# Kernel tuning notes

Measured on AMD Instinct MI355X. Metric: run time of the kernel, lower is better.

Reference implementation:

```python
import jax, jax.numpy as jnp
import numpy as np
import math
from jax import lax

DIM = 128
D_STATE = 16
D_CONV = 4
EXPAND = 2
NSLICES = 16
D_INNER = EXPAND * DIM          # 256
DT_RANK = math.ceil(DIM / 16)   # 8
B_, H_, W_ = 4, 64, 64
L = H_ * W_                     # 4096


def silu(x):
    return x * jax.nn.sigmoid(x)


def causal_conv1d(x, w, b):
    # x: (b, d, l), w: (d, k) depthwise, b: (d,)  -- causal, output length l
    l = x.shape[-1]
    xp = jnp.pad(x, ((0, 0), (0, 0), (D_CONV - 1, 0)))
    y = sum(w[None, :, k, None] * xp[:, :, k:k + l] for k in range(D_CONV))
    return y + b[None, :, None]


def selective_scan(u, delta, A, B, C):
    # u, delta: (b, d, l); A: (d, n); B, C: (b, n, l)
    bsz, d, l = u.shape
    n = A.shape[1]
    u_t = u.transpose(2, 0, 1)      # (l, b, d)
    d_t = delta.transpose(2, 0, 1)  # (l, b, d)
    B_t = B.transpose(2, 0, 1)      # (l, b, n)
    C_t = C.transpose(2, 0, 1)      # (l, b, n)

    def step(h, inp):
        u_, de_, b_, c_ = inp
        dA = jnp.exp(de_[..., None] * A)                    # (b, d, n)
        h = h * dA + (de_ * u_)[..., None] * b_[:, None, :]  # (b, d, n)
        y = jnp.einsum('bdn,bn->bd', h, c_)
        return h, y

    h0 = jnp.zeros((bsz, d, n), u.dtype)
    _, ys = lax.scan(step, h0, (u_t, d_t, B_t, C_t))
    return ys.transpose(1, 2, 0)  # (b, d, l)


def mamba_dir(xz, conv_w, conv_b, x_proj_w, dt_w, dt_b, A_log, Dp):
    # one directional Mamba branch (conv + S6 scan + silu(z) gating), returns (b, d_inner, l)
    x, z = jnp.split(xz, 2, axis=1)
    x = silu(causal_conv1d(x, conv_w, conv_b))
    x_dbl = jnp.einsum('rd,bdl->brl', x_proj_w, x)          # (b, dt_rank+2n, l)
    dt_raw = x_dbl[:, :DT_RANK]
    Bm = x_dbl[:, DT_RANK:DT_RANK + D_STATE]
    Cm = x_dbl[:, DT_RANK + D_STATE:]
    delta = jax.nn.softplus(jnp.einsum('dr,brl->bdl', dt_w, dt_raw) + dt_b[None, :, None])
    A = -jnp.exp(A_log)
    y = selective_scan(x, delta, A, Bm, Cm)
    y = y + Dp[None, :, None] * x
    return y * silu(z)


def setup_inputs() -> dict:
    key = jax.random.key(0)
    ks = iter(jax.random.split(key, 40))

    def rn(shape, scale=0.02):
        return jax.random.normal(next(ks), shape, dtype=jnp.float32) * scale

    inp = {"x_in": jax.random.normal(next(ks), (B_, H_, W_, DIM), dtype=jnp.float32)}
    inp["in_proj_w"] = rn((2 * D_INNER, DIM))
    for suf in ["", "_b", "_s"]:
        inp["conv_w" + suf] = rn((D_INNER, D_CONV), 0.1)
        inp["conv_b" + suf] = rn((D_INNER,), 0.1)
        inp["x_proj_w" + suf] = rn((DT_RANK + 2 * D_STATE, D_INNER))
        inp["dt_proj_w" + suf] = rn((D_INNER, DT_RANK), 0.1)
        inp["dt_proj_b" + suf] = rn((D_INNER,), 0.1)
        inp["A_log" + suf] = jnp.log(jnp.tile(jnp.arange(1, D_STATE + 1, dtype=jnp.float32), (D_INNER, 1)))
        inp["D" + suf] = jnp.ones((D_INNER,), jnp.float32)
    inp["out_proj_w"] = rn((DIM, D_INNER))
    return inp


def reference(x_in, in_proj_w, conv_w, conv_b, x_proj_w, dt_proj_w, dt_proj_b, A_log, D,
              conv_w_b, conv_b_b, x_proj_w_b, dt_proj_w_b, dt_proj_b_b, A_log_b, D_b,
              conv_w_s, conv_b_s, x_proj_w_s, dt_proj_w_s, dt_proj_b_s, A_log_s, D_s,
              out_proj_w):
    b, h, w, c = x_in.shape
    l = h * w
    x = x_in.reshape(b, l, c)
    xz = jnp.einsum('pd,bld->bpl', in_proj_w, x)  # (b, 2*d_inner, l)

    # forward scan
    y_f = mamba_dir(xz, conv_w, conv_b, x_proj_w, dt_proj_w, dt_proj_b, A_log, D)
    # backward scan (flip along length)
    y_b = jnp.flip(mamba_dir(jnp.flip(xz, -1), conv_w_b, conv_b_b, x_proj_w_b,
                             dt_proj_w_b, dt_proj_b_b, A_log_b, D_b), -1)
    # interleaved-slice scan: chunk length into NSLICES pieces, stack, flatten
    m = l // NSLICES
    xz_s = xz.reshape(b, 2 * D_INNER, NSLICES, m).swapaxes(-1, -2).reshape(b, 2 * D_INNER, l)
    y_s = mamba_dir(xz_s, conv_w_s, conv_b_s, x_proj_w_s, dt_proj_w_s, dt_proj_b_s, A_log_s, D_s)
    y_s = y_s.reshape(b, D_INNER, m, NSLICES).swapaxes(-1, -2).reshape(b, D_INNER, l)

    y = y_f + y_b + y_s
    out = jnp.einsum('od,bdl->blo', out_proj_w, y)
    return out.reshape(b, h, w, c)
```

## Files before the change

kernel.cpp:

```cpp
#include <hip/hip_runtime.h>
#include <math.h>

#define LSEQ 4096

#define XZ_OFF   0ULL
#define XZ_SZ    (4ULL * 4096 * 512)
#define U_OFF    (XZ_OFF + XZ_SZ)
#define DIR_SZ   (4ULL * 256 * 4096)
#define DELTA_OFF (U_OFF + 3ULL * DIR_SZ)
#define BC_OFF   (DELTA_OFF + 3ULL * DIR_SZ)
#define BC_SZ    (4ULL * 4096 * 32)
#define WTIN_OFF DELTA_OFF
#define WTOUT_OFF U_OFF

typedef float v2f __attribute__((ext_vector_type(2)));
typedef float v4f __attribute__((ext_vector_type(4)));

__device__ __forceinline__ float sigmoidf_(float x) { return 1.0f / (1.0f + __expf(-x)); }
__device__ __forceinline__ float siluf_(float x)    { return x * sigmoidf_(x); }

__device__ __forceinline__ float fast_exp2_asm(float x) {
    float r;
    asm volatile("v_exp_f32 %0, %1\n\ts_nop 0" : "=v"(r) : "v"(x));
    return r;
}
#if defined(__has_builtin)
#if __has_builtin(__builtin_amdgcn_exp2f)
#define EXP2(x) __builtin_amdgcn_exp2f(x)
#else
#define EXP2(x) fast_exp2_asm(x)
#endif
#else
#define EXP2(x) fast_exp2_asm(x)
#endif

__device__ __forceinline__ float softplus_fast(float x) {
    float t = EXP2(1.44269504f * x);
    float r = 0.69314718f * __log2f(1.0f + t);
    return (x > 20.0f) ? x : r;
}

__device__ __forceinline__ int perm_idx(int dir, int j) {
    if (dir == 0) return j;
    if (dir == 1) return 4095 - j;
    return ((j & 15) << 8) | (j >> 4);
}

#define DPP_MOV(x, ctrl) __int_as_float(__builtin_amdgcn_update_dpp(0, __float_as_int(x), (ctrl), 0xF, 0xF, true))

__global__ __launch_bounds__(256) void transpose_in_kernel(const float* __restrict__ w,
                                                           float* __restrict__ wT) {
    int idx = blockIdx.x * 256 + threadIdx.x;
    int p = idx >> 7, c = idx & 127;
    wT[(size_t)c * 512 + p] = w[(size_t)p * 128 + c];
}

__global__ __launch_bounds__(256) void inproj_kernel(const float* __restrict__ x,
                              const float* __restrict__ wT,
                              float* __restrict__ xz) {
    const int b = blockIdx.y;
    const int l0 = blockIdx.x * 16;
    __shared__ float xs[128 * 20];
    for (int idx = threadIdx.x; idx < 16 * 128; idx += 256) {
        int li = idx >> 7, c = idx & 127;
        xs[c * 20 + li] = x[((size_t)(b * 4096 + l0 + li)) * 128 + c];
    }
    __syncthreads();
    const int p0 = (threadIdx.x & 127) * 4;
    const int g8 = (threadIdx.x >> 7) * 8;
    float acc[4][8];
    #pragma unroll
    for (int j = 0; j < 4; ++j)
        #pragma unroll
        for (int k = 0; k < 8; ++k) acc[j][k] = 0.0f;
    for (int c = 0; c < 128; ++c) {
        float4 wv = *(const float4*)(wT + (size_t)c * 512 + p0);
        const float* xp = xs + c * 20 + g8;
        float4 x0 = *(const float4*)(xp);
        float4 x1 = *(const float4*)(xp + 4);
        float xv[8] = {x0.x, x0.y, x0.z, x0.w, x1.x, x1.y, x1.z, x1.w};
        float wj[4] = {wv.x, wv.y, wv.z, wv.w};
        #pragma unroll
        for (int j = 0; j < 4; ++j)
            #pragma unroll
            for (int k = 0; k < 8; ++k) acc[j][k] += wj[j] * xv[k];
    }
    #pragma unroll
    for (int k = 0; k < 8; ++k) {
        float4 s; s.x = acc[0][k]; s.y = acc[1][k]; s.z = acc[2][k]; s.w = acc[3][k];
        *(float4*)(xz + ((size_t)(b * 4096 + l0 + g8 + k)) * 512 + p0) = s;
    }
}

__global__ __launch_bounds__(256) void front_kernel(float* __restrict__ ws,
        const float* __restrict__ xw0, const float* __restrict__ xw1, const float* __restrict__ xw2,
        const float* __restrict__ dw0, const float* __restrict__ dw1, const float* __restrict__ dw2,
        const float* __restrict__ db0, const float* __restrict__ db1, const float* __restrict__ db2,
        const float* __restrict__ cw0, const float* __restrict__ cb0,
        const float* __restrict__ cw1, const float* __restrict__ cb1,
        const float* __restrict__ cw2, const float* __restrict__ cb2) {
    const int l0 = blockIdx.x * 32, b = blockIdx.y, dir = blockIdx.z;
    const float* xw = (dir == 0) ? xw0 : (dir == 1) ? xw1 : xw2;
    const float* dw = (dir == 0) ? dw0 : (dir == 1) ? dw1 : dw2;
    const float* db = (dir == 0) ? db0 : (dir == 1) ? db1 : db2;
    const float* cw = (dir == 0) ? cw0 : (dir == 1) ? cw1 : cw2;
    const float* cb = (dir == 0) ? cb0 : (dir == 1) ? cb1 : cb2;
    const float* xzb = ws + XZ_OFF + (size_t)b * 4096 * 512;
    float* ub      = ws + U_OFF + (size_t)dir * DIR_SZ + (size_t)b * 256 * 4096;
    float* deltab  = ws + DELTA_OFF + (size_t)dir * DIR_SZ + (size_t)b * 256 * 4096;
    float* Bf      = ws + BC_OFF + (size_t)dir * BC_SZ;
    float* Cf      = Bf + BC_SZ / 2;

    __shared__ float xt[35 * 260];
    __shared__ float xd[40 * 33];
    __shared__ float xws[40 * 68];
    float* ut = xt;

    for (int idx = threadIdx.x; idx < 35 * 64; idx += 256) {
        int k = idx >> 6, dq = idx & 63;
        int j = l0 - 3 + k;
        float4 v = {0.f, 0.f, 0.f, 0.f};
        if (j >= 0) {
            int row = (dir == 0) ? j : (dir == 1) ? (4095 - j) : (((j & 15) << 8) | (j >> 4));
            v = *(const float4*)(xzb + (size_t)row * 512 + dq * 4);
        }
        *(float4*)(xt + k * 260 + dq * 4) = v;
    }
    __syncthreads();

    const int d = threadIdx.x;
    const float w0 = cw[d * 4 + 0], w1 = cw[d * 4 + 1], w2 = cw[d * 4 + 2], w3 = cw[d * 4 + 3];
    const float bb = cb[d];
    float win[35];
    #pragma unroll
    for (int k = 0; k < 35; ++k) win[k] = xt[k * 260 + d];
    float r[32];
    #pragma unroll
    for (int li = 0; li < 32; ++li)
        r[li] = siluf_(bb + w0 * win[li] + w1 * win[li + 1] + w2 * win[li + 2] + w3 * win[li + 3]);
    {
        float* urow = ub + (size_t)d * 4096 + l0;
        #pragma unroll
        for (int q = 0; q < 8; ++q) {
            float4 v; v.x = r[q*4]; v.y = r[q*4+1]; v.z = r[q*4+2]; v.w = r[q*4+3];
            *(float4*)(urow + q * 4) = v;
        }
    }
    __syncthreads();

    #pragma unroll
    for (int li = 0; li < 32; ++li)
        ut[li * 264 + 4 * (((d >> 2) ^ (li & 7))) + (d & 3)] = r[li];

    {
        const int rg = threadIdx.x >> 5;
        const int li = threadIdx.x & 31;
        float acc[5];
        #pragma unroll
        for (int j = 0; j < 5; ++j) acc[j] = 0.0f;
        const float* up = ut + li * 264;
        const int sw = (li & 7);
        for (int ct = 0; ct < 4; ++ct) {
            __syncthreads();
            for (int idx = threadIdx.x; idx < 40 * 16; idx += 256) {
                int rr = idx >> 4, q = (idx & 15) * 4;
                *(float4*)(xws + rr * 68 + q) = *(const float4*)(xw + (size_t)rr * 256 + ct * 64 + q);
            }
            __syncthreads();
            #pragma unroll 4
            for (int c4t = 0; c4t < 16; ++c4t) {
                const int cc = 4 * (c4t ^ sw);
                float4 uv = *(const float4*)(up + ct * 64 + cc);
                #pragma unroll
                for (int j = 0; j < 5; ++j) {
                    float4 wv = *(const float4*)(xws + (rg * 5 + j) * 68 + cc);
                    acc[j] += wv.x * uv.x + wv.y * uv.y + wv.z * uv.z + wv.w * uv.w;
                }
            }
        }
        #pragma unroll
        for (int j = 0; j < 5; ++j) xd[(rg * 5 + j) * 33 + li] = acc[j];
    }
    __syncthreads();

    {
        const int wv = threadIdx.x >> 6;
        const int lane = threadIdx.x & 63;
        const int n = lane >> 2, lq = lane & 3;
        #pragma unroll
        for (int j = 0; j < 2; ++j) {
            int l4 = (l0 >> 2) + j * 4 + wv;
            int li = (j * 4 + wv) * 4 + lq;
            size_t base = (((size_t)b * 1024 + l4) * 16 + n) * 4 + lq;
            Bf[base] = xd[(8 + n) * 33 + li];
            Cf[base] = xd[(24 + n) * 33 + li];
        }
    }
    {
        const int li = threadIdx.x & 31;
        float xr8[8];
        #pragma unroll
        for (int rr = 0; rr < 8; ++rr) xr8[rr] = xd[rr * 33 + li];
        #pragma unroll
        for (int k = 0; k < 32; ++k) {
            int dd = ((threadIdx.x + k * 256) >> 5);
            float4 wa = *(const float4*)(dw + dd * 8);
            float4 wb = *(const float4*)(dw + dd * 8 + 4);
            float acc = db[dd]
                + wa.x * xr8[0] + wa.y * xr8[1] + wa.z * xr8[2] + wa.w * xr8[3]
                + wb.x * xr8[4] + wb.y * xr8[5] + wb.z * xr8[6] + wb.w * xr8[7];
            deltab[(size_t)dd * 4096 + l0 + li] = softplus_fast(acc);
        }
    }
}

__global__ __launch_bounds__(512) void scan_kernel(float* __restrict__ ws,
                            const float* __restrict__ Al0, const float* __restrict__ Dp0,
                            const float* __restrict__ Al1, const float* __restrict__ Dp1,
                            const float* __restrict__ Al2, const float* __restrict__ Dp2) {
    const int d = blockIdx.x, b = blockIdx.y, dir = blockIdx.z;
    const float* Al = (dir == 0) ? Al0 : (dir == 1) ? Al1 : Al2;
    const float* Dp = (dir == 0) ? Dp0 : (dir == 1) ? Dp1 : Dp2;
    const int c = threadIdx.x >> 4;
    const int n = threadIdx.x & 15;
    const int qid = n >> 2;
    const float Ane = -1.44269504f * __expf(Al[d * 16 + n]);
    const v2f AneD = {Ane, Ane};
    const float Dd = Dp[d];
    const float* urow = ws + U_OFF + (size_t)dir * DIR_SZ + ((size_t)(b * 256 + d)) * 4096;
    float* drow = ws + DELTA_OFF + (size_t)dir * DIR_SZ + ((size_t)(b * 256 + d)) * 4096;

    __shared__ float sdu[32 * 260];
    __shared__ float red[32 * 34];
    float* Psh = red;
    float* Ssh = red + 512;

    {
        const float4* d4 = (const float4*)drow;
        const float4* u4 = (const float4*)urow;
        for (int i = threadIdx.x; i < 1024; i += 512) {
            float4 dv = d4[i], uv = u4[i];
            int l = i * 4;
            float* p = sdu + (l >> 7) * 260 + (l & 127) * 2;
            float4 du;
            du.x = dv.x * uv.x; du.y = dv.y * uv.y; du.z = dv.z * uv.z; du.w = dv.w * uv.w;
            *(float4*)(p) = dv; *(float4*)(p + 4) = du;
        }
    }
    __syncthreads();

    const v4f* Bq = (const v4f*)(ws + BC_OFF + (size_t)dir * BC_SZ)
                       + ((size_t)b * 1024 + c * 32) * 16 + n;
    const v4f* Cq = (const v4f*)(ws + BC_OFF + (size_t)dir * BC_SZ + BC_SZ / 2)
                       + ((size_t)b * 1024 + c * 32) * 16 + n;
    const v4f* sp = (const v4f*)(sdu + c * 260);

    float S = 0.0f;
    v2f ds2 = {0.0f, 0.0f};
    #pragma unroll 8
    for (int k4 = 0; k4 < 32; ++k4) {
        v4f dq = sp[k4 * 2], uq = sp[k4 * 2 + 1];
        v4f Bv = Bq[(size_t)k4 * 16];
        v2f t0 = AneD * dq.xy;
        v2f t1 = AneD * dq.zw;
        v2f p0 = uq.xy * Bv.xy;
        v2f p1 = uq.zw * Bv.zw;
        ds2 += dq.xy + dq.zw;
        S = __builtin_fmaf(S, EXP2(t0.x), p0.x);
        S = __builtin_fmaf(S, EXP2(t0.y), p0.y);
        S = __builtin_fmaf(S, EXP2(t1.x), p1.x);
        S = __builtin_fmaf(S, EXP2(t1.y), p1.y);
    }
    Ssh[c * 16 + n] = S;
    Psh[c * 16 + n] = EXP2(Ane * (ds2.x + ds2.y));
    __syncthreads();
    float h = 0.0f;
    for (int k = 0; k < c; ++k) h = h * Psh[k * 16 + n] + Ssh[k * 16 + n];
    __syncthreads();

    #define SCAN_STEP(t, ee, pp, Cn) { \
        h = __builtin_fmaf(h, (ee), (pp)); \
        float yp = h * (Cn); \
        yp += DPP_MOV(yp, 0xB1); \
        yp += DPP_MOV(yp, 0x4E); \
        red[(4 * (t) + qid) * 34 + c] = yp; }

    for (int g = 0; g < 16; ++g) {
        v4f d0 = sp[g * 4 + 0], u0 = sp[g * 4 + 1];
        v4f d1 = sp[g * 4 + 2], u1 = sp[g * 4 + 3];
        v4f Bv0 = Bq[(size_t)(g * 2) * 16], Bv1 = Bq[(size_t)(g * 2 + 1) * 16];
        v4f Cv0 = Cq[(size_t)(g * 2) * 16], Cv1 = Cq[(size_t)(g * 2 + 1) * 16];
        v2f t0 = AneD * d0.xy, t1 = AneD * d0.zw;
        v2f t2 = AneD * d1.xy, t3 = AneD * d1.zw;
        v2f p0 = u0.xy * Bv0.xy, p1 = u0.zw * Bv0.zw;
        v2f p2 = u1.xy * Bv1.xy, p3 = u1.zw * Bv1.zw;
        float e0 = EXP2(t0.x), e1 = EXP2(t0.y);
        float e2 = EXP2(t1.x), e3 = EXP2(t1.y);
        float e4 = EXP2(t2.x), e5 = EXP2(t2.y);
        float e6 = EXP2(t3.x), e7 = EXP2(t3.y);
        SCAN_STEP(0, e0, p0.x, Cv0.x)
        SCAN_STEP(1, e1, p0.y, Cv0.y)
        SCAN_STEP(2, e2, p1.x, Cv0.z)
        SCAN_STEP(3, e3, p1.y, Cv0.w)
        SCAN_STEP(4, e4, p2.x, Cv1.x)
        SCAN_STEP(5, e5, p2.y, Cv1.y)
        SCAN_STEP(6, e6, p3.x, Cv1.z)
        SCAN_STEP(7, e7, p3.y, Cv1.w)
        const int tt = n & 7;
        float q0 = red[(4 * tt + 0) * 34 + c];
        float q1 = red[(4 * tt + 1) * 34 + c];
        float q2 = red[(4 * tt + 2) * 34 + c];
        float q3 = red[(4 * tt + 3) * 34 + c];
        float y = (q0 + q1) + (q2 + q3);
        if (n < 8) {
            int gl = c * 128 + g * 8 + n;
            drow[perm_idx(dir, gl)] = y + Dd * urow[gl];
        }
    }
    #undef SCAN_STEP
}

__global__ __launch_bounds__(256) void transpose_w_kernel(const float* __restrict__ ow,
                                                          float* __restrict__ wT) {
    int idx = blockIdx.x * 256 + threadIdx.x;
    int o = idx >> 8, d = idx & 255;
    wT[(size_t)d * 128 + o] = ow[(size_t)o * 256 + d];
}

__global__ __launch_bounds__(256) void epilogue_kernel(const float* __restrict__ ws,
                                const float* __restrict__ wT,
                                float* __restrict__ out) {
    const int l0 = blockIdx.x * 16, b = blockIdx.y;
    __shared__ float yt[256 * 20];
    __shared__ float wts[64 * 128];
    const float* yf = ws + DELTA_OFF;
    const float* yb = ws + DELTA_OFF + DIR_SZ;
    const float* ysd = ws + DELTA_OFF + 2 * DIR_SZ;
    const float* xzb = ws + XZ_OFF + (size_t)b * 4096 * 512;

    for (int idx = threadIdx.x; idx < 256 * 4; idx += 256) {
        int d = idx >> 2, q = (idx & 3) * 4;
        size_t ro = ((size_t)(b * 256 + d)) * 4096 + l0 + q;
        float4 vf = *(const float4*)(yf + ro);
        float4 vb = *(const float4*)(yb + ro);
        float4 vs = *(const float4*)(ysd + ro);
        float4 s; s.x = vf.x + vb.x + vs.x; s.y = vf.y + vb.y + vs.y;
        s.z = vf.z + vb.z + vs.z; s.w = vf.w + vb.w + vs.w;
        *(float4*)(yt + d * 20 + q) = s;
    }
    __syncthreads();
    {
        const int d = threadIdx.x;
        #pragma unroll 4
        for (int li = 0; li < 16; ++li) {
            float z = xzb[(size_t)(l0 + li) * 512 + 256 + d];
            yt[d * 20 + li] *= siluf_(z);
        }
    }

    const int o0 = (threadIdx.x & 31) * 4;
    const int lp = (threadIdx.x >> 5) * 2;
    float a0[4], a1[4];
    #pragma unroll
    for (int j = 0; j < 4; ++j) { a0[j] = 0.0f; a1[j] = 0.0f; }
    for (int dt = 0; dt < 4; ++dt) {
        __syncthreads();
        for (int idx = threadIdx.x; idx < 64 * 32; idx += 256) {
            int dd = idx >> 5, q = (idx & 31) * 4;
            *(float4*)(wts + dd * 128 + q) = *(const float4*)(wT + (size_t)(dt * 64 + dd) * 128 + q);
        }
        __syncthreads();
        #pragma unroll 4
        for (int dl = 0; dl < 64; ++dl) {
            float4 w = *(const float4*)(wts + dl * 128 + o0);
            float2 y = *(const float2*)(yt + (dt * 64 + dl) * 20 + lp);
            a0[0] += w.x * y.x; a0[1] += w.y * y.x; a0[2] += w.z * y.x; a0[3] += w.w * y.x;
            a1[0] += w.x * y.y; a1[1] += w.y * y.y; a1[2] += w.z * y.y; a1[3] += w.w * y.y;
        }
    }
    float4 s0; s0.x = a0[0]; s0.y = a0[1]; s0.z = a0[2]; s0.w = a0[3];
    float4 s1; s1.x = a1[0]; s1.y = a1[1]; s1.z = a1[2]; s1.w = a1[3];
    *(float4*)(out + ((size_t)(b * 4096 + l0 + lp)) * 128 + o0) = s0;
    *(float4*)(out + ((size_t)(b * 4096 + l0 + lp + 1)) * 128 + o0) = s1;
}

extern "C" void kernel_launch(void* const* d_in, const int* in_sizes, int n_in,
                              void* d_out, int out_size, void* d_ws, size_t ws_size,
                              hipStream_t stream) {
    const float* x_in = (const float*)d_in[0];
    const float* ipw  = (const float*)d_in[1];
    const float* cw[3]  = {(const float*)d_in[2],  (const float*)d_in[9],  (const float*)d_in[16]};
    const float* cb[3]  = {(const float*)d_in[3],  (const float*)d_in[10], (const float*)d_in[17]};
    const float* xpw[3] = {(const float*)d_in[4],  (const float*)d_in[11], (const float*)d_in[18]};
    const float* dtw[3] = {(const float*)d_in[5],  (const float*)d_in[12], (const float*)d_in[19]};
    const float* dtb[3] = {(const float*)d_in[6],  (const float*)d_in[13], (const float*)d_in[20]};
    const float* alog[3]= {(const float*)d_in[7],  (const float*)d_in[14], (const float*)d_in[21]};
    const float* dp[3]  = {(const float*)d_in[8],  (const float*)d_in[15], (const float*)d_in[22]};
    const float* ow   = (const float*)d_in[23];
    float* ws  = (float*)d_ws;
    float* out = (float*)d_out;

    transpose_in_kernel<<<dim3(256), 256, 0, stream>>>(ipw, ws + WTIN_OFF);
    inproj_kernel<<<dim3(256, 4), 256, 0, stream>>>(x_in, ws + WTIN_OFF, ws);
    front_kernel<<<dim3(128, 4, 3), 256, 0, stream>>>(ws,
        xpw[0], xpw[1], xpw[2], dtw[0], dtw[1], dtw[2], dtb[0], dtb[1], dtb[2],
        cw[0], cb[0], cw[1], cb[1], cw[2], cb[2]);
    scan_kernel<<<dim3(256, 4, 3), 512, 0, stream>>>(ws,
        alog[0], dp[0], alog[1], dp[1], alog[2], dp[2]);
    transpose_w_kernel<<<dim3(128), 256, 0, stream>>>(ow, ws + WTOUT_OFF);
    epilogue_kernel<<<dim3(256, 4), 256, 0, stream>>>(ws, ws + WTOUT_OFF, out);
}
```

Baseline: 379.0 us.

## Replace LDS reduction in scan with full DPP row reduction and lane select

In the scan kernel the sum over the 16 state lanes now uses four DPP adds instead of writing partial sums to a shared reduction buffer and reading them back. Each lane keeps the output for its own timestep in a register, so the shared buffer and the barrier after the chunk-prefix loop can be removed. The kernel also stores raw u rather than delta*u in LDS and reads u for the skip term from LDS instead of global memory, with a minimum-blocks hint added to launch bounds. The cost is extra DPP and multiply work per step, which is traded for fewer LDS accesses and less synchronisation.

```diff
diff --git a/kernel.cpp b/kernel.cpp
--- a/kernel.cpp
+++ b/kernel.cpp
@@ -214,7 +214,7 @@
     }
 }
 
-__global__ __launch_bounds__(512) void scan_kernel(float* __restrict__ ws,
+__global__ __launch_bounds__(512, 8) void scan_kernel(float* __restrict__ ws,
                             const float* __restrict__ Al0, const float* __restrict__ Dp0,
                             const float* __restrict__ Al1, const float* __restrict__ Dp1,
                             const float* __restrict__ Al2, const float* __restrict__ Dp2) {
@@ -223,7 +223,7 @@
     const float* Dp = (dir == 0) ? Dp0 : (dir == 1) ? Dp1 : Dp2;
     const int c = threadIdx.x >> 4;
     const int n = threadIdx.x & 15;
-    const int qid = n >> 2;
+    const int nl = n & 7;
     const float Ane = -1.44269504f * __expf(Al[d * 16 + n]);
     const v2f AneD = {Ane, Ane};
     const float Dd = Dp[d];
@@ -231,9 +231,9 @@
     float* drow = ws + DELTA_OFF + (size_t)dir * DIR_SZ + ((size_t)(b * 256 + d)) * 4096;
 
     __shared__ float sdu[32 * 260];
-    __shared__ float red[32 * 34];
-    float* Psh = red;
-    float* Ssh = red + 512;
+    __shared__ float ps[1024];
+    float* Psh = ps;
+    float* Ssh = ps + 512;
 
     {
         const float4* d4 = (const float4*)drow;
@@ -242,9 +242,7 @@
             float4 dv = d4[i], uv = u4[i];
             int l = i * 4;
             float* p = sdu + (l >> 7) * 260 + (l & 127) * 2;
-            float4 du;
-            du.x = dv.x * uv.x; du.y = dv.y * uv.y; du.z = dv.z * uv.z; du.w = dv.w * uv.w;
-            *(float4*)(p) = dv; *(float4*)(p + 4) = du;
+            *(float4*)(p) = dv; *(float4*)(p + 4) = uv;
         }
     }
     __syncthreads();
@@ -261,10 +259,12 @@
     for (int k4 = 0; k4 < 32; ++k4) {
         v4f dq = sp[k4 * 2], uq = sp[k4 * 2 + 1];
         v4f Bv = Bq[(size_t)k4 * 16];
+        v2f du0 = dq.xy * uq.xy;
+        v2f du1 = dq.zw * uq.zw;
         v2f t0 = AneD * dq.xy;
         v2f t1 = AneD * dq.zw;
-        v2f p0 = uq.xy * Bv.xy;
-        v2f p1 = uq.zw * Bv.zw;
+        v2f p0 = du0 * Bv.xy;
+        v2f p1 = du1 * Bv.zw;
         ds2 += dq.xy + dq.zw;
         S = __builtin_fmaf(S, EXP2(t0.x), p0.x);
         S = __builtin_fmaf(S, EXP2(t0.y), p0.y);
@@ -275,29 +275,36 @@
     Psh[c * 16 + n] = EXP2(Ane * (ds2.x + ds2.y));
     __syncthreads();
     float h = 0.0f;
-    for (int k = 0; k < c; ++k) h = h * Psh[k * 16 + n] + Ssh[k * 16 + n];
-    __syncthreads();
+    #pragma unroll 2
+    for (int k = 0; k < c; ++k) h = __builtin_fmaf(h, Psh[k * 16 + n], Ssh[k * 16 + n]);
 
     #define SCAN_STEP(t, ee, pp, Cn) { \
         h = __builtin_fmaf(h, (ee), (pp)); \
         float yp = h * (Cn); \
         yp += DPP_MOV(yp, 0xB1); \
         yp += DPP_MOV(yp, 0x4E); \
-        red[(4 * (t) + qid) * 34 + c] = yp; }
+        yp += DPP_MOV(yp, 0x124); \
+        yp += DPP_MOV(yp, 0x128); \
+        if (nl == (t)) ysel = yp; }
 
     for (int g = 0; g < 16; ++g) {
+        const int j0 = g * 8 + nl;
+        float uo = sdu[c * 260 + ((j0 >> 2) << 3) + 4 + (j0 & 3)];
         v4f d0 = sp[g * 4 + 0], u0 = sp[g * 4 + 1];
         v4f d1 = sp[g * 4 + 2], u1 = sp[g * 4 + 3];
         v4f Bv0 = Bq[(size_t)(g * 2) * 16], Bv1 = Bq[(size_t)(g * 2 + 1) * 16];
         v4f Cv0 = Cq[(size_t)(g * 2) * 16], Cv1 = Cq[(size_t)(g * 2 + 1) * 16];
         v2f t0 = AneD * d0.xy, t1 = AneD * d0.zw;
         v2f t2 = AneD * d1.xy, t3 = AneD * d1.zw;
-        v2f p0 = u0.xy * Bv0.xy, p1 = u0.zw * Bv0.zw;
-        v2f p2 = u1.xy * Bv1.xy, p3 = u1.zw * Bv1.zw;
+        v2f q0 = d0.xy * u0.xy, q1 = d0.zw * u0.zw;
+        v2f q2 = d1.xy * u1.xy, q3 = d1.zw * u1.zw;
+        v2f p0 = q0 * Bv0.xy, p1 = q1 * Bv0.zw;
+        v2f p2 = q2 * Bv1.xy, p3 = q3 * Bv1.zw;
         float e0 = EXP2(t0.x), e1 = EXP2(t0.y);
         float e2 = EXP2(t1.x), e3 = EXP2(t1.y);
         float e4 = EXP2(t2.x), e5 = EXP2(t2.y);
         float e6 = EXP2(t3.x), e7 = EXP2(t3.y);
+        float ysel = 0.0f;
         SCAN_STEP(0, e0, p0.x, Cv0.x)
         SCAN_STEP(1, e1, p0.y, Cv0.y)
         SCAN_STEP(2, e2, p1.x, Cv0.z)
@@ -306,16 +313,7 @@
         SCAN_STEP(5, e5, p2.y, Cv1.y)
         SCAN_STEP(6, e6, p3.x, Cv1.z)
         SCAN_STEP(7, e7, p3.y, Cv1.w)
-        const int tt = n & 7;
-        float q0 = red[(4 * tt + 0) * 34 + c];
-        float q1 = red[(4 * tt + 1) * 34 + c];
-        float q2 = red[(4 * tt + 2) * 34 + c];
-        float q3 = red[(4 * tt + 3) * 34 + c];
-        float y = (q0 + q1) + (q2 + q3);
-        if (n < 8) {
-            int gl = c * 128 + g * 8 + n;
-            drow[perm_idx(dir, gl)] = y + Dd * urow[gl];
-        }
+        if (n < 8) drow[perm_idx(dir, c * 128 + j0)] = ysel + Dd * uo;
     }
     #undef SCAN_STEP
 }
```

Result: faster. 361.0 us (-4.7%).
